# Kernel optimization log

Measured on AMD Instinct MI355X. Metric: run time of the kernel, lower is better.

Reference implementation:

```python
import jax, jax.numpy as jnp
import numpy as np

IN_DIM = 512
OUT_DIM = 512
NUM_HARMONICS = 32
BATCH = 4096


def setup_inputs() -> dict:
    key = jax.random.key(0)
    k1, k2 = jax.random.split(key)
    x = jax.random.normal(k1, (BATCH, IN_DIM), dtype=jnp.float32)
    std = 1.0 / np.sqrt(IN_DIM * NUM_HARMONICS)
    fourier_coeffs = jax.random.normal(
        k2, (IN_DIM, NUM_HARMONICS, 2, OUT_DIM), dtype=jnp.float32) * std
    bias = jnp.zeros((OUT_DIM,), dtype=jnp.float32)
    return {"x": x, "fourier_coeffs": fourier_coeffs, "bias": bias}


def reference(x, fourier_coeffs, bias):
    # k = [1, ..., num_harmonics]
    k = jnp.arange(1, fourier_coeffs.shape[1] + 1, dtype=x.dtype)
    kx = x[:, :, None] * k                      # [b, i, g]
    trig = jnp.stack([jnp.cos(kx), jnp.sin(kx)], axis=-1)  # [b, i, g, 2]
    out = jnp.einsum('bigf,igfo->bo', trig, fourier_coeffs)
    return out + bias
```

## Files before the change

kernel.cpp:

```cpp
#include <hip/hip_runtime.h>
#include <hip/hip_bf16.h>
#include <stdint.h>
#include <stddef.h>

#define BATCH   4096
#define INDIM   512
#define OUTDIM  512
#define NH      32
#define KKDIM   64
#define INV2PI  0.15915494309189535f

#define BM       128
#define BN       256
#define THREADS  512
#define KSPLIT   4
#define DIMS_PER_WG (INDIM / KSPLIT)
#define CHUNK_ELEMS (BN * KKDIM)

#define B_BYTES   32768
#define A_STRIDE  72
#define A_BYTES   (BM * A_STRIDE * 2)
#define OFF_A0    (2 * B_BYTES)
#define OFF_X     (OFF_A0 + 2 * A_BYTES)
#define SMEM_BYTES (OFF_X + 2 * 8 * 128 * 4)

typedef short  bhalf8  __attribute__((ext_vector_type(8)));
typedef float  vfloat4 __attribute__((ext_vector_type(4)));

__device__ __forceinline__ unsigned pack_bf16(float a, float b) {
    union { __hip_bfloat162 h2; unsigned u; } cv;
    cv.h2 = __float22bfloat162_rn(float2{a, b});
    return cv.u;
}

__device__ __forceinline__ void async_copy16(const void* gsrc, void* ldst) {
    __builtin_amdgcn_global_load_lds(
        (const __attribute__((address_space(1))) void*)(uintptr_t)gsrc,
        (__attribute__((address_space(3))) void*)(uint32_t)(uintptr_t)ldst,
        16, 0, 0);
}

__global__ __launch_bounds__(256) void fkan_prepass(const float* __restrict__ coeffs,
                                                    unsigned short* __restrict__ Bt) {
    const int t  = threadIdx.x;
    const int cb = blockIdx.x & 1;
    const int i  = blockIdx.x >> 1;
    const float* __restrict__ src = coeffs + (size_t)i * (KKDIM * OUTDIM) + cb * BN;
    unsigned short* __restrict__ chunk = Bt + (size_t)(cb * INDIM + i) * CHUNK_ELEMS;
#pragma unroll
    for (int s = 0; s < 8; ++s) {
        const int unit = t + s * 256;
        const int col  = unit >> 3;
        const int pc   = unit & 7;
        const int kb   = (pc ^ (col & 7)) * 8;
        const float* p0 = src + (size_t)kb * OUTDIM + col;
        uint4 o;
        o.x = pack_bf16(p0[0 * OUTDIM], p0[1 * OUTDIM]);
        o.y = pack_bf16(p0[2 * OUTDIM], p0[3 * OUTDIM]);
        o.z = pack_bf16(p0[4 * OUTDIM], p0[5 * OUTDIM]);
        o.w = pack_bf16(p0[6 * OUTDIM], p0[7 * OUTDIM]);
        ((uint4*)chunk)[unit] = o;
    }
}

__global__ __launch_bounds__(256) void fkan_bias_init(const float* __restrict__ bias,
                                                      float* __restrict__ out) {
    const int idx = blockIdx.x * 256 + threadIdx.x;
    ((float4*)out)[idx] = ((const float4*)bias)[idx & 127];
}

__device__ __forceinline__ void stage_B(const unsigned short* __restrict__ Bt, char* smem,
                                        int cb, int dim_global, int parity, int t) {
    const char* chunk = (const char*)(Bt + (size_t)(cb * INDIM + dim_global) * CHUNK_ELEMS);
    char* bdst = smem + parity * B_BYTES;
#pragma unroll
    for (int s = 0; s < 4; ++s) {
        const int unit = t + s * 512;
        async_copy16(chunk + unit * 16, bdst + unit * 16);
    }
}

__device__ __forceinline__ void stage_x(const float* __restrict__ x, char* smem,
                                        int rowbase, int dimbase, int cn, int t) {
    const int r  = t >> 2;
    const int d0 = (t & 3) * 2;
    const float2 xv = *(const float2*)(x + (size_t)(rowbase + r) * INDIM + dimbase + cn * 8 + d0);
    float* xr = (float*)(smem + OFF_X + (cn & 1) * 4096);
    xr[(d0 + 0) * 128 + r] = xv.x * INV2PI;
    xr[(d0 + 1) * 128 + r] = xv.y * INV2PI;
}

__device__ __forceinline__ void do_trig(char* smem, int dim_local, int parity, int trow, int tq) {
    const float rv = ((const float*)(smem + OFF_X + ((dim_local >> 3) & 1) * 4096))
                     [(dim_local & 7) * 128 + trow];
    const float cd = __builtin_amdgcn_cosf(rv);
    const float sd = __builtin_amdgcn_sinf(rv);
    const float a0 = (float)(tq * 8 + 1) * rv;
    float c = __builtin_amdgcn_cosf(a0);
    float s = __builtin_amdgcn_sinf(a0);
    unsigned pk[8];
    pk[0] = pack_bf16(c, s);
#pragma unroll
    for (int j = 1; j < 8; ++j) {
        const float nc = c * cd - s * sd;
        const float ns = s * cd + c * sd;
        c = nc; s = ns;
        pk[j] = pack_bf16(c, s);
    }
    uint4* adst = (uint4*)(smem + OFF_A0 + parity * A_BYTES + trow * (A_STRIDE * 2) + tq * 32);
    uint4 w0; w0.x = pk[0]; w0.y = pk[1]; w0.z = pk[2]; w0.w = pk[3];
    uint4 w1; w1.x = pk[4]; w1.y = pk[5]; w1.z = pk[6]; w1.w = pk[7];
    adst[0] = w0;
    adst[1] = w1;
}

__global__ __launch_bounds__(THREADS, 2) void fkan_main(const float* __restrict__ x,
                                                        const unsigned short* __restrict__ Bt,
                                                        float* __restrict__ out) {
    __shared__ char smem[SMEM_BYTES];
    const int t      = threadIdx.x;
    const int grp    = blockIdx.x & 7;
    const int member = blockIdx.x >> 3;
    const int cb      = grp & 1;
    const int kq      = grp >> 1;
    const int rowbase = member * BM;
    const int colbase = cb * BN;
    const int dimbase = kq * DIMS_PER_WG;

    const int lane = t & 63;
    const int w    = t >> 6;
    const int wr   = w >> 2;
    const int wc   = w & 3;
    const int fr   = lane & 15;
    const int fq   = lane >> 4;
    const int fx   = lane & 7;

    const int trow = t & 127;
    const int tq   = t >> 7;

    vfloat4 acc[4][4];
#pragma unroll
    for (int a = 0; a < 4; ++a)
#pragma unroll
        for (int b = 0; b < 4; ++b) acc[a][b] = (vfloat4)0.0f;

    stage_x(x, smem, rowbase, dimbase, 0, t);
    __syncthreads();
    stage_B(Bt, smem, cb, dimbase + 0, 0, t);
    do_trig(smem, 0, 0, trow, tq);
    __syncthreads();

#pragma unroll 2
    for (int it = 0; it < DIMS_PER_WG; ++it) {
        const int p    = it & 1;
        const int inxt = it + 1;
        if (inxt < DIMS_PER_WG) {
            stage_B(Bt, smem, cb, dimbase + inxt, inxt & 1, t);
            if ((it & 7) == 0) {
                const int cn = (it >> 3) + 1;
                if (cn < 16) stage_x(x, smem, rowbase, dimbase, cn, t);
            }
            do_trig(smem, inxt, inxt & 1, trow, tq);
        }
        {
            const char* Ab = smem + OFF_A0 + p * A_BYTES;
            const char* Bb = smem + p * B_BYTES;
#pragma unroll
            for (int ks = 0; ks < 2; ++ks) {
                bhalf8 av[4], bv[4];
#pragma unroll
                for (int rt = 0; rt < 4; ++rt)
                    av[rt] = *(const bhalf8*)(Ab + (wr * 64 + rt * 16 + fr) * (A_STRIDE * 2)
                                                 + ks * 64 + fq * 16);
#pragma unroll
                for (int ct = 0; ct < 4; ++ct)
                    bv[ct] = *(const bhalf8*)(Bb + (wc * 64 + ct * 16 + fr) * 128
                                                 + (((ks * 4 + fq) ^ fx) * 16));
#pragma unroll
                for (int rt = 0; rt < 4; ++rt)
#pragma unroll
                    for (int ct = 0; ct < 4; ++ct)
                        acc[rt][ct] = __builtin_amdgcn_mfma_f32_16x16x32_bf16(
                            av[rt], bv[ct], acc[rt][ct], 0, 0, 0);
            }
        }
        __syncthreads();
    }

#pragma unroll
    for (int rt = 0; rt < 4; ++rt) {
#pragma unroll
        for (int ct = 0; ct < 4; ++ct) {
            const int col  = colbase + wc * 64 + ct * 16 + fr;
            const int row0 = rowbase + wr * 64 + rt * 16 + fq * 4;
#pragma unroll
            for (int r = 0; r < 4; ++r)
                atomicAdd(out + (size_t)(row0 + r) * OUTDIM + col, acc[rt][ct][r]);
        }
    }
}

__global__ __launch_bounds__(256) void fkan_naive(const float* __restrict__ x,
                                                  const float* __restrict__ coeffs,
                                                  const float* __restrict__ bias,
                                                  float* __restrict__ out) {
    const int b = blockIdx.x >> 1;
    const int o = ((blockIdx.x & 1) << 8) + threadIdx.x;
    float acc = bias[o];
    const float* xrow = x + (size_t)b * INDIM;
    for (int i = 0; i < INDIM; ++i) {
        const float rv = xrow[i] * INV2PI;
        const float cd = __builtin_amdgcn_cosf(rv);
        const float sd = __builtin_amdgcn_sinf(rv);
        float c = cd, s = sd;
        const float* cp = coeffs + (size_t)i * (KKDIM * OUTDIM) + o;
#pragma unroll 4
        for (int g = 0; g < NH; ++g) {
            acc += c * cp[g * 2 * OUTDIM] + s * cp[(g * 2 + 1) * OUTDIM];
            const float nc = c * cd - s * sd;
            const float ns = s * cd + c * sd;
            c = nc; s = ns;
        }
    }
    out[(size_t)b * OUTDIM + o] = acc;
}

extern "C" void kernel_launch(void* const* d_in, const int* in_sizes, int n_in,
                              void* d_out, int out_size, void* d_ws, size_t ws_size,
                              hipStream_t stream) {
    (void)in_sizes; (void)n_in; (void)out_size;
    const float* x      = (const float*)d_in[0];
    const float* coeffs = (const float*)d_in[1];
    const float* bias   = (const float*)d_in[2];
    float* out          = (float*)d_out;

    const size_t bt_bytes = (size_t)2 * INDIM * CHUNK_ELEMS * sizeof(unsigned short);
    if (ws_size >= bt_bytes) {
        unsigned short* Bt = (unsigned short*)d_ws;
        fkan_prepass<<<2 * INDIM, 256, 0, stream>>>(coeffs, Bt);
        fkan_bias_init<<<(BATCH * OUTDIM) / (4 * 256), 256, 0, stream>>>(bias, out);
        fkan_main<<<(BATCH / BM) * 2 * KSPLIT, THREADS, 0, stream>>>(x, Bt, out);
    } else {
        fkan_naive<<<BATCH * 2, 256, 0, stream>>>(x, coeffs, bias, out);
    }
}
```

Measured before the change: 293.1 us.

## Load B fragments directly into registers and shrink tiles to 128x128

The main kernel no longer stages coefficient chunks through LDS with async global-to-LDS copies. Each wave now loads its B fragments from global memory straight into a double-buffered register set, one dimension ahead. Workgroups drop to 256 threads on a 128x128 tile, with each thread computing 16 harmonics in the trig step. The prepass is rewritten to read coalesced float4 rows and transpose them through LDS into an unswizzled layout. This frees LDS and removes B-tile LDS traffic, but adds global-load latency exposure and more register pressure. It also doubles the number of workgroups that recompute the same trig values per column block.

```diff
diff --git a/kernel.cpp b/kernel.cpp
--- a/kernel.cpp
+++ b/kernel.cpp
@@ -11,18 +11,17 @@
 #define INV2PI  0.15915494309189535f
 
 #define BM       128
-#define BN       256
-#define THREADS  512
+#define BN       128
+#define THREADS  256
 #define KSPLIT   4
 #define DIMS_PER_WG (INDIM / KSPLIT)
+#define NCOLB    (OUTDIM / BN)
 #define CHUNK_ELEMS (BN * KKDIM)
 
-#define B_BYTES   32768
-#define A_STRIDE  72
-#define A_BYTES   (BM * A_STRIDE * 2)
-#define OFF_A0    (2 * B_BYTES)
-#define OFF_X     (OFF_A0 + 2 * A_BYTES)
-#define SMEM_BYTES (OFF_X + 2 * 8 * 128 * 4)
+#define A_STRIDE 72
+#define A_BYTES  (BM * A_STRIDE * 2)
+#define OFF_X    (2 * A_BYTES)
+#define SMEM_BYTES (OFF_X + 2 * 8 * BM * 4)
 
 typedef short  bhalf8  __attribute__((ext_vector_type(8)));
 typedef float  vfloat4 __attribute__((ext_vector_type(4)));
@@ -33,33 +32,38 @@
     return cv.u;
 }
 
-__device__ __forceinline__ void async_copy16(const void* gsrc, void* ldst) {
-    __builtin_amdgcn_global_load_lds(
-        (const __attribute__((address_space(1))) void*)(uintptr_t)gsrc,
-        (__attribute__((address_space(3))) void*)(uint32_t)(uintptr_t)ldst,
-        16, 0, 0);
-}
-
 __global__ __launch_bounds__(256) void fkan_prepass(const float* __restrict__ coeffs,
                                                     unsigned short* __restrict__ Bt) {
-    const int t  = threadIdx.x;
-    const int cb = blockIdx.x & 1;
-    const int i  = blockIdx.x >> 1;
-    const float* __restrict__ src = coeffs + (size_t)i * (KKDIM * OUTDIM) + cb * BN;
-    unsigned short* __restrict__ chunk = Bt + (size_t)(cb * INDIM + i) * CHUNK_ELEMS;
+    __shared__ unsigned short tl[BN * 76];
+    const int t   = threadIdx.x;
+    const int cb  = blockIdx.x & 3;
+    const int dim = blockIdx.x >> 2;
+    const float* __restrict__ src = coeffs + (size_t)dim * (KKDIM * OUTDIM) + cb * BN;
+#pragma unroll
+    for (int s = 0; s < 2; ++s) {
+        const int idx = t + s * 256;
+        const int kq  = idx >> 5;
+        const int c4  = (idx & 31) * 4;
+        float4 f[4];
+#pragma unroll
+        for (int r = 0; r < 4; ++r)
+            f[r] = *(const float4*)(src + (size_t)(kq * 4 + r) * OUTDIM + c4);
+#pragma unroll
+        for (int k = 0; k < 4; ++k) {
+            uint2 w;
+            w.x = pack_bf16(((const float*)&f[0])[k], ((const float*)&f[1])[k]);
+            w.y = pack_bf16(((const float*)&f[2])[k], ((const float*)&f[3])[k]);
+            *(uint2*)(tl + (c4 + k) * 76 + kq * 4) = w;
+        }
+    }
+    __syncthreads();
+    uint2* __restrict__ dst = (uint2*)(Bt + ((size_t)cb * INDIM + dim) * CHUNK_ELEMS);
 #pragma unroll
     for (int s = 0; s < 8; ++s) {
         const int unit = t + s * 256;
-        const int col  = unit >> 3;
-        const int pc   = unit & 7;
-        const int kb   = (pc ^ (col & 7)) * 8;
-        const float* p0 = src + (size_t)kb * OUTDIM + col;
-        uint4 o;
-        o.x = pack_bf16(p0[0 * OUTDIM], p0[1 * OUTDIM]);
-        o.y = pack_bf16(p0[2 * OUTDIM], p0[3 * OUTDIM]);
-        o.z = pack_bf16(p0[4 * OUTDIM], p0[5 * OUTDIM]);
-        o.w = pack_bf16(p0[6 * OUTDIM], p0[7 * OUTDIM]);
-        ((uint4*)chunk)[unit] = o;
+        const int col  = unit >> 4;
+        const int s4   = unit & 15;
+        dst[unit] = *(const uint2*)(tl + col * 76 + s4 * 4);
     }
 }
 
@@ -69,75 +73,113 @@
     ((float4*)out)[idx] = ((const float4*)bias)[idx & 127];
 }
 
-__device__ __forceinline__ void stage_B(const unsigned short* __restrict__ Bt, char* smem,
-                                        int cb, int dim_global, int parity, int t) {
-    const char* chunk = (const char*)(Bt + (size_t)(cb * INDIM + dim_global) * CHUNK_ELEMS);
-    char* bdst = smem + parity * B_BYTES;
-#pragma unroll
-    for (int s = 0; s < 4; ++s) {
-        const int unit = t + s * 512;
-        async_copy16(chunk + unit * 16, bdst + unit * 16);
-    }
-}
-
 __device__ __forceinline__ void stage_x(const float* __restrict__ x, char* smem,
                                         int rowbase, int dimbase, int cn, int t) {
-    const int r  = t >> 2;
-    const int d0 = (t & 3) * 2;
-    const float2 xv = *(const float2*)(x + (size_t)(rowbase + r) * INDIM + dimbase + cn * 8 + d0);
+    const int r  = t >> 1;
+    const int d0 = (t & 1) * 4;
+    const float4 xv = *(const float4*)(x + (size_t)(rowbase + r) * INDIM + dimbase + cn * 8 + d0);
     float* xr = (float*)(smem + OFF_X + (cn & 1) * 4096);
-    xr[(d0 + 0) * 128 + r] = xv.x * INV2PI;
-    xr[(d0 + 1) * 128 + r] = xv.y * INV2PI;
+    xr[(d0 + 0) * BM + r] = xv.x * INV2PI;
+    xr[(d0 + 1) * BM + r] = xv.y * INV2PI;
+    xr[(d0 + 2) * BM + r] = xv.z * INV2PI;
+    xr[(d0 + 3) * BM + r] = xv.w * INV2PI;
 }
 
 __device__ __forceinline__ void do_trig(char* smem, int dim_local, int parity, int trow, int tq) {
     const float rv = ((const float*)(smem + OFF_X + ((dim_local >> 3) & 1) * 4096))
-                     [(dim_local & 7) * 128 + trow];
+                     [(dim_local & 7) * BM + trow];
     const float cd = __builtin_amdgcn_cosf(rv);
     const float sd = __builtin_amdgcn_sinf(rv);
-    const float a0 = (float)(tq * 8 + 1) * rv;
+    const float a0 = (float)(tq * 16 + 1) * rv;
     float c = __builtin_amdgcn_cosf(a0);
     float s = __builtin_amdgcn_sinf(a0);
-    unsigned pk[8];
+    unsigned pk[16];
     pk[0] = pack_bf16(c, s);
 #pragma unroll
-    for (int j = 1; j < 8; ++j) {
+    for (int j = 1; j < 16; ++j) {
         const float nc = c * cd - s * sd;
         const float ns = s * cd + c * sd;
         c = nc; s = ns;
         pk[j] = pack_bf16(c, s);
     }
-    uint4* adst = (uint4*)(smem + OFF_A0 + parity * A_BYTES + trow * (A_STRIDE * 2) + tq * 32);
-    uint4 w0; w0.x = pk[0]; w0.y = pk[1]; w0.z = pk[2]; w0.w = pk[3];
-    uint4 w1; w1.x = pk[4]; w1.y = pk[5]; w1.z = pk[6]; w1.w = pk[7];
-    adst[0] = w0;
-    adst[1] = w1;
+    uint4* adst = (uint4*)(smem + parity * A_BYTES + trow * (A_STRIDE * 2) + tq * 64);
+#pragma unroll
+    for (int q = 0; q < 4; ++q) {
+        uint4 w; w.x = pk[q * 4]; w.y = pk[q * 4 + 1]; w.z = pk[q * 4 + 2]; w.w = pk[q * 4 + 3];
+        adst[q] = w;
+    }
+}
+
+template <int P>
+__device__ __forceinline__ void fkan_step(int it, const float* __restrict__ x,
+                                          const unsigned short* __restrict__ chunk0,
+                                          char* smem, int rowbase, int dimbase,
+                                          const int (&boff)[8],
+                                          bhalf8 (&cur)[8], bhalf8 (&nxt)[8],
+                                          vfloat4 (&acc)[4][4],
+                                          int t, int wr, int wc, int fr, int fq,
+                                          int trow, int tq) {
+    const int inxt = it + 1;
+    if (inxt < DIMS_PER_WG) {
+        const unsigned short* ch = chunk0 + (size_t)inxt * CHUNK_ELEMS;
+#pragma unroll
+        for (int j = 0; j < 8; ++j)
+            nxt[j] = *(const bhalf8*)(ch + boff[j]);
+        if ((it & 7) == 0) {
+            const int cn = (it >> 3) + 1;
+            if (cn < 16) stage_x(x, smem, rowbase, dimbase, cn, t);
+        }
+        do_trig(smem, inxt, P ^ 1, trow, tq);
+    }
+    const char* Ab = smem + P * A_BYTES;
+#pragma unroll
+    for (int ks = 0; ks < 2; ++ks) {
+        bhalf8 av[4];
+#pragma unroll
+        for (int rt = 0; rt < 4; ++rt)
+            av[rt] = *(const bhalf8*)(Ab + (wr * 64 + rt * 16 + fr) * (A_STRIDE * 2)
+                                         + ks * 64 + fq * 16);
+#pragma unroll
+        for (int rt = 0; rt < 4; ++rt)
+#pragma unroll
+            for (int ct = 0; ct < 4; ++ct)
+                acc[rt][ct] = __builtin_amdgcn_mfma_f32_16x16x32_bf16(
+                    av[rt], cur[ks * 4 + ct], acc[rt][ct], 0, 0, 0);
+    }
+    __syncthreads();
 }
 
 __global__ __launch_bounds__(THREADS, 2) void fkan_main(const float* __restrict__ x,
                                                         const unsigned short* __restrict__ Bt,
                                                         float* __restrict__ out) {
     __shared__ char smem[SMEM_BYTES];
-    const int t      = threadIdx.x;
-    const int grp    = blockIdx.x & 7;
-    const int member = blockIdx.x >> 3;
-    const int cb      = grp & 1;
-    const int kq      = grp >> 1;
+    const int t       = threadIdx.x;
+    const int grp     = blockIdx.x & 15;
+    const int member  = blockIdx.x >> 4;
+    const int cb      = grp & 3;
+    const int kq      = grp >> 2;
     const int rowbase = member * BM;
     const int colbase = cb * BN;
     const int dimbase = kq * DIMS_PER_WG;
 
     const int lane = t & 63;
     const int w    = t >> 6;
-    const int wr   = w >> 2;
-    const int wc   = w & 3;
+    const int wr   = w >> 1;
+    const int wc   = w & 1;
     const int fr   = lane & 15;
     const int fq   = lane >> 4;
-    const int fx   = lane & 7;
 
     const int trow = t & 127;
     const int tq   = t >> 7;
 
+    const unsigned short* chunk0 = Bt + ((size_t)cb * INDIM + dimbase) * CHUNK_ELEMS;
+    int boff[8];
+#pragma unroll
+    for (int ks = 0; ks < 2; ++ks)
+#pragma unroll
+        for (int ct = 0; ct < 4; ++ct)
+            boff[ks * 4 + ct] = (wc * 64 + ct * 16 + fr) * KKDIM + (ks * 4 + fq) * 8;
+
     vfloat4 acc[4][4];
 #pragma unroll
     for (int a = 0; a < 4; ++a)
@@ -146,45 +188,18 @@
 
     stage_x(x, smem, rowbase, dimbase, 0, t);
     __syncthreads();
-    stage_B(Bt, smem, cb, dimbase + 0, 0, t);
     do_trig(smem, 0, 0, trow, tq);
-    __syncthreads();
-
-#pragma unroll 2
-    for (int it = 0; it < DIMS_PER_WG; ++it) {
-        const int p    = it & 1;
-        const int inxt = it + 1;
-        if (inxt < DIMS_PER_WG) {
-            stage_B(Bt, smem, cb, dimbase + inxt, inxt & 1, t);
-            if ((it & 7) == 0) {
-                const int cn = (it >> 3) + 1;
-                if (cn < 16) stage_x(x, smem, rowbase, dimbase, cn, t);
-            }
-            do_trig(smem, inxt, inxt & 1, trow, tq);
-        }
-        {
-            const char* Ab = smem + OFF_A0 + p * A_BYTES;
-            const char* Bb = smem + p * B_BYTES;
-#pragma unroll
-            for (int ks = 0; ks < 2; ++ks) {
-                bhalf8 av[4], bv[4];
-#pragma unroll
-                for (int rt = 0; rt < 4; ++rt)
-                    av[rt] = *(const bhalf8*)(Ab + (wr * 64 + rt * 16 + fr) * (A_STRIDE * 2)
-                                                 + ks * 64 + fq * 16);
-#pragma unroll
-                for (int ct = 0; ct < 4; ++ct)
-                    bv[ct] = *(const bhalf8*)(Bb + (wc * 64 + ct * 16 + fr) * 128
-                                                 + (((ks * 4 + fq) ^ fx) * 16));
-#pragma unroll
-                for (int rt = 0; rt < 4; ++rt)
-#pragma unroll
-                    for (int ct = 0; ct < 4; ++ct)
-                        acc[rt][ct] = __builtin_amdgcn_mfma_f32_16x16x32_bf16(
-                            av[rt], bv[ct], acc[rt][ct], 0, 0, 0);
-            }
-        }
-        __syncthreads();
+    bhalf8 bv0[8], bv1[8];
+#pragma unroll
+    for (int j = 0; j < 8; ++j)
+        bv0[j] = *(const bhalf8*)(chunk0 + boff[j]);
+    __syncthreads();
+
+    for (int it = 0; it < DIMS_PER_WG; it += 2) {
+        fkan_step<0>(it,     x, chunk0, smem, rowbase, dimbase, boff, bv0, bv1, acc,
+                     t, wr, wc, fr, fq, trow, tq);
+        fkan_step<1>(it + 1, x, chunk0, smem, rowbase, dimbase, boff, bv1, bv0, acc,
+                     t, wr, wc, fr, fq, trow, tq);
     }
 
 #pragma unroll
@@ -234,12 +249,12 @@
     const float* bias   = (const float*)d_in[2];
     float* out          = (float*)d_out;
 
-    const size_t bt_bytes = (size_t)2 * INDIM * CHUNK_ELEMS * sizeof(unsigned short);
+    const size_t bt_bytes = (size_t)NCOLB * INDIM * CHUNK_ELEMS * sizeof(unsigned short);
     if (ws_size >= bt_bytes) {
         unsigned short* Bt = (unsigned short*)d_ws;
-        fkan_prepass<<<2 * INDIM, 256, 0, stream>>>(coeffs, Bt);
+        fkan_prepass<<<NCOLB * INDIM, 256, 0, stream>>>(coeffs, Bt);
         fkan_bias_init<<<(BATCH * OUTDIM) / (4 * 256), 256, 0, stream>>>(bias, out);
-        fkan_main<<<(BATCH / BM) * 2 * KSPLIT, THREADS, 0, stream>>>(x, Bt, out);
+        fkan_main<<<(BATCH / BM) * NCOLB * KSPLIT, THREADS, 0, stream>>>(x, Bt, out);
     } else {
         fkan_naive<<<BATCH * 2, 256, 0, stream>>>(x, coeffs, bias, out);
     }
```

After: 361.9 us. +23.5%, slower.

## Generate trig fragments in registers and switch to 32x32 MFMA with two-dim B stages

Applied to the files above, without the earlier changes.

The main kernel stops writing the cos/sin A operand to shared memory. Each lane now computes its A fragments directly in registers, using angle doubling and recurrences, one dim ahead of use. It switches from 16x16x32 to 32x32x16 bf16 MFMA, stages B for two dims per period with a 64KB double buffer, and syncs once per two dims instead of every dim. The prepass now uses float4 loads and transposes through shared memory for coalesced writes. In exchange, each lane recomputes trig values that several waves share, register pressure rises, and shared memory use grows to about 128KB, which may limit occupancy at two blocks per CU.

```diff
diff --git a/kernel.cpp b/kernel.cpp
--- a/kernel.cpp
+++ b/kernel.cpp
@@ -15,17 +15,15 @@
 #define THREADS  512
 #define KSPLIT   4
 #define DIMS_PER_WG (INDIM / KSPLIT)
+#define PERIODS  (DIMS_PER_WG / 2)
 #define CHUNK_ELEMS (BN * KKDIM)
-
-#define B_BYTES   32768
-#define A_STRIDE  72
-#define A_BYTES   (BM * A_STRIDE * 2)
-#define OFF_A0    (2 * B_BYTES)
-#define OFF_X     (OFF_A0 + 2 * A_BYTES)
-#define SMEM_BYTES (OFF_X + 2 * 8 * 128 * 4)
-
-typedef short  bhalf8  __attribute__((ext_vector_type(8)));
-typedef float  vfloat4 __attribute__((ext_vector_type(4)));
+#define CHUNK_BYTES (CHUNK_ELEMS * 2)
+
+#define OFF_XS     131072
+#define SMEM_BYTES (OFF_XS + 2 * 8 * BM * 4)
+
+typedef short  bhalf8   __attribute__((ext_vector_type(8)));
+typedef float  vfloat16 __attribute__((ext_vector_type(16)));
 
 __device__ __forceinline__ unsigned pack_bf16(float a, float b) {
     union { __hip_bfloat162 h2; unsigned u; } cv;
@@ -42,24 +40,39 @@
 
 __global__ __launch_bounds__(256) void fkan_prepass(const float* __restrict__ coeffs,
                                                     unsigned short* __restrict__ Bt) {
-    const int t  = threadIdx.x;
-    const int cb = blockIdx.x & 1;
-    const int i  = blockIdx.x >> 1;
-    const float* __restrict__ src = coeffs + (size_t)i * (KKDIM * OUTDIM) + cb * BN;
-    unsigned short* __restrict__ chunk = Bt + (size_t)(cb * INDIM + i) * CHUNK_ELEMS;
+    __shared__ char tl[32768];
+    const int t   = threadIdx.x;
+    const int cb  = blockIdx.x & 1;
+    const int dim = blockIdx.x >> 1;
+    const float* __restrict__ src = coeffs + (size_t)dim * (KKDIM * OUTDIM) + cb * BN;
+#pragma unroll
+    for (int s = 0; s < 2; ++s) {
+        const int idx = t + s * 256;
+        const int u   = idx >> 6;
+        const int c4  = (idx & 63) * 4;
+        float4 f[8];
+#pragma unroll
+        for (int j = 0; j < 8; ++j)
+            f[j] = *(const float4*)(src + (size_t)(u * 8 + j) * OUTDIM + c4);
+        const float* fp = (const float*)f;
+#pragma unroll
+        for (int i = 0; i < 4; ++i) {
+            const int col = c4 + i;
+            uint4 o;
+            o.x = pack_bf16(fp[0 * 4 + i], fp[1 * 4 + i]);
+            o.y = pack_bf16(fp[2 * 4 + i], fp[3 * 4 + i]);
+            o.z = pack_bf16(fp[4 * 4 + i], fp[5 * 4 + i]);
+            o.w = pack_bf16(fp[6 * 4 + i], fp[7 * 4 + i]);
+            *(uint4*)(tl + col * 128 + (u ^ (col & 7)) * 16) = o;
+        }
+    }
+    __syncthreads();
+    uint4* __restrict__ dst = (uint4*)(Bt + ((size_t)cb * INDIM + dim) * CHUNK_ELEMS);
+    const uint4* tls = (const uint4*)tl;
 #pragma unroll
     for (int s = 0; s < 8; ++s) {
         const int unit = t + s * 256;
-        const int col  = unit >> 3;
-        const int pc   = unit & 7;
-        const int kb   = (pc ^ (col & 7)) * 8;
-        const float* p0 = src + (size_t)kb * OUTDIM + col;
-        uint4 o;
-        o.x = pack_bf16(p0[0 * OUTDIM], p0[1 * OUTDIM]);
-        o.y = pack_bf16(p0[2 * OUTDIM], p0[3 * OUTDIM]);
-        o.z = pack_bf16(p0[4 * OUTDIM], p0[5 * OUTDIM]);
-        o.w = pack_bf16(p0[6 * OUTDIM], p0[7 * OUTDIM]);
-        ((uint4*)chunk)[unit] = o;
+        dst[unit] = tls[unit];
     }
 }
 
@@ -69,58 +82,80 @@
     ((float4*)out)[idx] = ((const float4*)bias)[idx & 127];
 }
 
-__device__ __forceinline__ void stage_B(const unsigned short* __restrict__ Bt, char* smem,
-                                        int cb, int dim_global, int parity, int t) {
-    const char* chunk = (const char*)(Bt + (size_t)(cb * INDIM + dim_global) * CHUNK_ELEMS);
-    char* bdst = smem + parity * B_BYTES;
-#pragma unroll
-    for (int s = 0; s < 4; ++s) {
-        const int unit = t + s * 512;
-        async_copy16(chunk + unit * 16, bdst + unit * 16);
+__device__ __forceinline__ void stage_B2(const unsigned short* __restrict__ chunk0,
+                                         char* smem, int d0, int bufq, int t) {
+    const char* src = (const char*)chunk0 + (size_t)d0 * CHUNK_BYTES;
+    char* dst = smem + bufq * 65536;
+#pragma unroll
+    for (int r = 0; r < 8; ++r) {
+        const int off = (r * 512 + t) * 16;
+        async_copy16(src + off, dst + off);
     }
 }
 
 __device__ __forceinline__ void stage_x(const float* __restrict__ x, char* smem,
-                                        int rowbase, int dimbase, int cn, int t) {
-    const int r  = t >> 2;
-    const int d0 = (t & 3) * 2;
-    const float2 xv = *(const float2*)(x + (size_t)(rowbase + r) * INDIM + dimbase + cn * 8 + d0);
-    float* xr = (float*)(smem + OFF_X + (cn & 1) * 4096);
-    xr[(d0 + 0) * 128 + r] = xv.x * INV2PI;
-    xr[(d0 + 1) * 128 + r] = xv.y * INV2PI;
-}
-
-__device__ __forceinline__ void do_trig(char* smem, int dim_local, int parity, int trow, int tq) {
-    const float rv = ((const float*)(smem + OFF_X + ((dim_local >> 3) & 1) * 4096))
-                     [(dim_local & 7) * 128 + trow];
-    const float cd = __builtin_amdgcn_cosf(rv);
-    const float sd = __builtin_amdgcn_sinf(rv);
-    const float a0 = (float)(tq * 8 + 1) * rv;
-    float c = __builtin_amdgcn_cosf(a0);
-    float s = __builtin_amdgcn_sinf(a0);
-    unsigned pk[8];
-    pk[0] = pack_bf16(c, s);
-#pragma unroll
-    for (int j = 1; j < 8; ++j) {
-        const float nc = c * cd - s * sd;
-        const float ns = s * cd + c * sd;
-        c = nc; s = ns;
-        pk[j] = pack_bf16(c, s);
-    }
-    uint4* adst = (uint4*)(smem + OFF_A0 + parity * A_BYTES + trow * (A_STRIDE * 2) + tq * 32);
-    uint4 w0; w0.x = pk[0]; w0.y = pk[1]; w0.z = pk[2]; w0.w = pk[3];
-    uint4 w1; w1.x = pk[4]; w1.y = pk[5]; w1.z = pk[6]; w1.w = pk[7];
-    adst[0] = w0;
-    adst[1] = w1;
+                                        int rowbase, int dimbase, int c, int t) {
+    const int r  = t & 127;
+    const int dp = t >> 7;
+    const float2 xv = *(const float2*)(x + (size_t)(rowbase + r) * INDIM + dimbase + c * 8 + dp * 2);
+    float* xr = (float*)(smem + OFF_XS + (c & 1) * 4096);
+    xr[(dp * 2 + 0) * BM + r] = xv.x * INV2PI;
+    xr[(dp * 2 + 1) * BM + r] = xv.y * INV2PI;
+}
+
+__device__ __forceinline__ void gen_row(float tr, int half, unsigned (&pk)[16]) {
+    const float c1 = __builtin_amdgcn_cosf(tr);
+    const float s1 = __builtin_amdgcn_sinf(tr);
+    const float c2 = c1 * c1 - s1 * s1, s2 = 2.f * c1 * s1;
+    const float c4 = c2 * c2 - s2 * s2, s4 = 2.f * c2 * s2;
+    const float c8 = c4 * c4 - s4 * s4, s8 = 2.f * c4 * s4;
+    const float c5 = c1 * c4 - s1 * s4, s5 = s1 * c4 + c1 * s4;
+    float fc = half ? c5 : c1;
+    float fs = half ? s5 : s1;
+#pragma unroll
+    for (int ks = 0; ks < 4; ++ks) {
+        float gc = fc, gs = fs;
+        pk[ks * 4 + 0] = pack_bf16(gc, gs);
+#pragma unroll
+        for (int j = 1; j < 4; ++j) {
+            const float nc = gc * c1 - gs * s1;
+            const float ns = gs * c1 + gc * s1;
+            gc = nc; gs = ns;
+            pk[ks * 4 + j] = pack_bf16(gc, gs);
+        }
+        if (ks < 3) {
+            const float nc = fc * c8 - fs * s8;
+            const float ns = fs * c8 + fc * s8;
+            fc = nc; fs = ns;
+        }
+    }
+}
+
+__device__ __forceinline__ void gen_dim(const char* smem, int dn, int lrow0, int half,
+                                        bhalf8 (&dst)[2][4]) {
+    const float* xs = (const float*)(smem + OFF_XS + ((dn >> 3) & 1) * 4096) + (dn & 7) * BM;
+#pragma unroll
+    for (int rt = 0; rt < 2; ++rt) {
+        const float tr = xs[lrow0 + rt * 32];
+        unsigned pk[16];
+        gen_row(tr, half, pk);
+#pragma unroll
+        for (int ks = 0; ks < 4; ++ks) {
+            union { unsigned u[4]; bhalf8 v; } cv;
+            cv.u[0] = pk[ks * 4 + 0]; cv.u[1] = pk[ks * 4 + 1];
+            cv.u[2] = pk[ks * 4 + 2]; cv.u[3] = pk[ks * 4 + 3];
+            dst[rt][ks] = cv.v;
+        }
+    }
 }
 
 __global__ __launch_bounds__(THREADS, 2) void fkan_main(const float* __restrict__ x,
                                                         const unsigned short* __restrict__ Bt,
                                                         float* __restrict__ out) {
     __shared__ char smem[SMEM_BYTES];
-    const int t      = threadIdx.x;
-    const int grp    = blockIdx.x & 7;
-    const int member = blockIdx.x >> 3;
+    const int t       = threadIdx.x;
+    const int grp     = blockIdx.x & 7;
+    const int member  = blockIdx.x >> 3;
     const int cb      = grp & 1;
     const int kq      = grp >> 1;
     const int rowbase = member * BM;
@@ -131,71 +166,75 @@
     const int w    = t >> 6;
     const int wr   = w >> 2;
     const int wc   = w & 3;
-    const int fr   = lane & 15;
-    const int fq   = lane >> 4;
-    const int fx   = lane & 7;
-
-    const int trow = t & 127;
-    const int tq   = t >> 7;
-
-    vfloat4 acc[4][4];
-#pragma unroll
-    for (int a = 0; a < 4; ++a)
-#pragma unroll
-        for (int b = 0; b < 4; ++b) acc[a][b] = (vfloat4)0.0f;
+    const int l31  = lane & 31;
+    const int half = lane >> 5;
+    const int lrow0 = wr * 64 + l31;
+
+    const unsigned short* chunk0 = Bt + ((size_t)cb * INDIM + dimbase) * CHUNK_ELEMS;
+
+    int coladdr[2], ksoff[4];
+#pragma unroll
+    for (int ct = 0; ct < 2; ++ct) coladdr[ct] = (wc * 64 + ct * 32 + l31) * 128;
+#pragma unroll
+    for (int ks = 0; ks < 4; ++ks) ksoff[ks] = ((ks * 2 + half) ^ (lane & 7)) * 16;
+
+    vfloat16 acc[2][2];
+#pragma unroll
+    for (int a = 0; a < 2; ++a)
+#pragma unroll
+        for (int b = 0; b < 2; ++b) acc[a][b] = (vfloat16)0.0f;
+
+    bhalf8 areg[2][2][4];
 
     stage_x(x, smem, rowbase, dimbase, 0, t);
+    stage_B2(chunk0, smem, 0, 0, t);
     __syncthreads();
-    stage_B(Bt, smem, cb, dimbase + 0, 0, t);
-    do_trig(smem, 0, 0, trow, tq);
-    __syncthreads();
-
-#pragma unroll 2
-    for (int it = 0; it < DIMS_PER_WG; ++it) {
-        const int p    = it & 1;
-        const int inxt = it + 1;
-        if (inxt < DIMS_PER_WG) {
-            stage_B(Bt, smem, cb, dimbase + inxt, inxt & 1, t);
-            if ((it & 7) == 0) {
-                const int cn = (it >> 3) + 1;
-                if (cn < 16) stage_x(x, smem, rowbase, dimbase, cn, t);
+    gen_dim(smem, 0, lrow0, half, areg[0]);
+
+    for (int p = 0; p < PERIODS; ++p) {
+        const int q = p & 1;
+        if ((p & 3) == 2) {
+            const int c = (p + 2) >> 2;
+            if (c < 16) stage_x(x, smem, rowbase, dimbase, c, t);
+        }
+        if (p < PERIODS - 1)
+            stage_B2(chunk0, smem, 2 * p + 2, 1 - q, t);
+
+#pragma unroll
+        for (int h = 0; h < 2; ++h) {
+            const int d = 2 * p + h;
+            const char* bb = smem + q * 65536 + h * 32768;
+            bhalf8 bv[2][4];
+#pragma unroll
+            for (int ks = 0; ks < 4; ++ks)
+#pragma unroll
+                for (int ct = 0; ct < 2; ++ct)
+                    bv[ct][ks] = *(const bhalf8*)(bb + coladdr[ct] + ksoff[ks]);
+            if (d + 1 < DIMS_PER_WG)
+                gen_dim(smem, d + 1, lrow0, half, areg[1 - h]);
+#pragma unroll
+            for (int ks = 0; ks < 4; ++ks)
+#pragma unroll
+                for (int rt = 0; rt < 2; ++rt)
+#pragma unroll
+                    for (int ct = 0; ct < 2; ++ct)
+                        acc[rt][ct] = __builtin_amdgcn_mfma_f32_32x32x16_bf16(
+                            areg[h][rt][ks], bv[ct][ks], acc[rt][ct], 0, 0, 0);
+        }
+        __syncthreads();
+    }
+
+#pragma unroll
+    for (int rt = 0; rt < 2; ++rt) {
+#pragma unroll
+        for (int ct = 0; ct < 2; ++ct) {
+            const int col   = colbase + wc * 64 + ct * 32 + l31;
+            const int rbase = rowbase + wr * 64 + rt * 32 + 4 * half;
+#pragma unroll
+            for (int reg = 0; reg < 16; ++reg) {
+                const int row = rbase + (reg & 3) + 8 * (reg >> 2);
+                atomicAdd(out + (size_t)row * OUTDIM + col, acc[rt][ct][reg]);
             }
-            do_trig(smem, inxt, inxt & 1, trow, tq);
-        }
-        {
-            const char* Ab = smem + OFF_A0 + p * A_BYTES;
-            const char* Bb = smem + p * B_BYTES;
-#pragma unroll
-            for (int ks = 0; ks < 2; ++ks) {
-                bhalf8 av[4], bv[4];
-#pragma unroll
-                for (int rt = 0; rt < 4; ++rt)
-                    av[rt] = *(const bhalf8*)(Ab + (wr * 64 + rt * 16 + fr) * (A_STRIDE * 2)
-                                                 + ks * 64 + fq * 16);
-#pragma unroll
-                for (int ct = 0; ct < 4; ++ct)
-                    bv[ct] = *(const bhalf8*)(Bb + (wc * 64 + ct * 16 + fr) * 128
-                                                 + (((ks * 4 + fq) ^ fx) * 16));
-#pragma unroll
-                for (int rt = 0; rt < 4; ++rt)
-#pragma unroll
-                    for (int ct = 0; ct < 4; ++ct)
-                        acc[rt][ct] = __builtin_amdgcn_mfma_f32_16x16x32_bf16(
-                            av[rt], bv[ct], acc[rt][ct], 0, 0, 0);
-            }
-        }
-        __syncthreads();
-    }
-
-#pragma unroll
-    for (int rt = 0; rt < 4; ++rt) {
-#pragma unroll
-        for (int ct = 0; ct < 4; ++ct) {
-            const int col  = colbase + wc * 64 + ct * 16 + fr;
-            const int row0 = rowbase + wr * 64 + rt * 16 + fq * 4;
-#pragma unroll
-            for (int r = 0; r < 4; ++r)
-                atomicAdd(out + (size_t)(row0 + r) * OUTDIM + col, acc[rt][ct][r]);
         }
     }
 }
```

After: 354.8 us. 1.21x slower.
